# Optimization experiments

Measured on AMD Instinct MI355X. Metric: run time of the kernel, lower is better.

Reference implementation:

```python
import jax, jax.numpy as jnp
import numpy as np

N_ATOMS = 16384
APC = 64            # atoms per conformer
N_CONF = 256        # 64 mols * 4 confs
N_MOL = 64
DEG = 32
E = N_ATOMS * DEG
H = 128             # hidden_channels = num_filters = out_channels
G = 50              # num_gaussians
L = 6               # num_interactions
CUTOFF = 10.0
LOG2 = float(np.log(2.0))


def ssp(x):
    # ShiftedSoftplus: softplus(x) - log(2)
    return jax.nn.softplus(x) - LOG2


def setup_inputs() -> dict:
    key = jax.random.key(0)
    ks = jax.random.split(key, 24)
    rng = np.random.default_rng(0)

    z = jnp.asarray(rng.integers(1, 100, size=(N_ATOMS,)), dtype=jnp.int64 if jax.config.jax_enable_x64 else jnp.int32)
    # positions uniform in a 5A box -> all intra-conformer distances < cutoff
    pos = jax.random.uniform(ks[0], (N_ATOMS, 3), dtype=jnp.float32) * 5.0

    # within-conformer random edges, no self loops (radius_graph surrogate)
    i = np.repeat(np.arange(N_ATOMS), DEG)
    off = rng.integers(1, APC, size=E)
    j = (i // APC) * APC + (i % APC + off) % APC
    edge_index = jnp.asarray(np.stack([j, i]), dtype=jnp.int32)  # [2,E] (source, target)

    atom_to_conf = jnp.asarray(np.arange(N_ATOMS) // APC, dtype=jnp.int32)
    conf_to_mol = jnp.asarray(np.arange(N_CONF) // (N_CONF // N_MOL), dtype=jnp.int32)

    s = 0.05
    p = {
        'emb':     jax.random.normal(ks[1], (120, H), jnp.float32) * s,
        # per-interaction stacked params [L, ...]
        'mlp_w1':  jax.random.normal(ks[2], (L, G, H), jnp.float32) * s,
        'mlp_b1':  jnp.zeros((L, H), jnp.float32),
        'mlp_w2':  jax.random.normal(ks[3], (L, H, H), jnp.float32) * s,
        'mlp_b2':  jnp.zeros((L, H), jnp.float32),
        'cf_w1':   jax.random.normal(ks[4], (L, H, H), jnp.float32) * s,
        'cf_w2':   jax.random.normal(ks[5], (L, H, H), jnp.float32) * s,
        'cf_b2':   jnp.zeros((L, H), jnp.float32),
        'int_w':   jax.random.normal(ks[6], (L, H, H), jnp.float32) * s,
        'int_b':   jnp.zeros((L, H), jnp.float32),
        # readout head
        'out_w1':  jax.random.normal(ks[7], (H, H), jnp.float32) * s,
        'out_b1':  jnp.zeros((H,), jnp.float32),
        'out_w2':  jax.random.normal(ks[8], (H, H), jnp.float32) * s,
        'out_b2':  jnp.zeros((H,), jnp.float32),
        'head_w1': jax.random.normal(ks[9], (H, H // 2), jnp.float32) * s,
        'head_b1': jnp.zeros((H // 2,), jnp.float32),
        'head_w2': jax.random.normal(ks[10], (H // 2, 1), jnp.float32) * s,
        'head_b2': jnp.zeros((1,), jnp.float32),
    }
    return dict(z=z, pos=pos, edge_index=edge_index, atom_to_conf=atom_to_conf,
                conf_to_mol=conf_to_mol, **p)


def reference(z, pos, edge_index, atom_to_conf, conf_to_mol, emb,
              mlp_w1, mlp_b1, mlp_w2, mlp_b2, cf_w1, cf_w2, cf_b2,
              int_w, int_b, out_w1, out_b1, out_w2, out_b2,
              head_w1, head_b1, head_w2, head_b2):
    row, col = edge_index[0], edge_index[1]  # message from row, aggregated at col

    h = emb[z]                                             # [N,H]
    edge_weight = jnp.linalg.norm(pos[row] - pos[col], axis=-1)  # [E]

    # GaussianSmearing
    offset = jnp.linspace(0.0, CUTOFF, G)
    coeff = -0.5 / (offset[1] - offset[0]) ** 2
    edge_attr = jnp.exp(coeff * (edge_weight[:, None] - offset[None, :]) ** 2)  # [E,G]

    C = 0.5 * (jnp.cos(edge_weight * jnp.pi / CUTOFF) + 1.0)  # cosine cutoff [E]

    for l in range(L):
        # filter network on edge features, modulated by cutoff envelope
        Wf = ssp(edge_attr @ mlp_w1[l] + mlp_b1[l]) @ mlp_w2[l] + mlp_b2[l]
        Wf = Wf * C[:, None]                               # [E,H]
        xf = h @ cf_w1[l]                                  # lin1 (no bias) [N,H]
        msg = xf[row] * Wf                                 # gather * filter [E,H]
        agg = jax.ops.segment_sum(msg, col, num_segments=N_ATOMS)  # scatter-add [N,H]
        xc = agg @ cf_w2[l] + cf_b2[l]                     # lin2
        h = h + (ssp(xc) @ int_w[l] + int_b[l])            # act, lin, residual

    h = ssp(h @ out_w1 + out_b1)
    h = h @ out_w2 + out_b2                                # [N,H]

    conf_emb = jax.ops.segment_sum(h, atom_to_conf, num_segments=N_CONF)   # [C,H]
    mol_emb = jax.ops.segment_sum(conf_emb, conf_to_mol, num_segments=N_MOL)  # [M,H]

    out = (ssp(mol_emb @ head_w1 + head_b1) @ head_w2 + head_b2)[:, 0]  # [M]
    return out
```

## Files before the change

kernel.cpp:

```cpp
#include <hip/hip_runtime.h>
#include <math.h>

#define N_ATOMS 16384
#define APC 64
#define N_CONF 256
#define N_MOL 64
#define DEG 32
#define NEDGE (N_ATOMS * DEG)
#define H 128
#define G 50
#define NL 6
#define TP0 512
#define TPB 4096
#define CUTOFF 10.0f

typedef __attribute__((ext_vector_type(8))) short short8_t;
typedef __attribute__((ext_vector_type(4))) float f32x4;
typedef __attribute__((ext_vector_type(2))) float f32x2;

__device__ __forceinline__ float ssp_f(float x) {
  float e = __expf(-fabsf(x));
  return fmaxf(x, 0.f) + __logf(1.f + e) - 0.69314718055994531f;
}
__device__ __forceinline__ unsigned short bf16_rne(float x) {
  unsigned u = __float_as_uint(x);
  unsigned r = u + 0x7FFF + ((u >> 16) & 1);
  return (unsigned short)(r >> 16);
}
__device__ __forceinline__ float bf16_to_f(unsigned short s) {
  return __uint_as_float(((unsigned)s) << 16);
}
__device__ __forceinline__ float bflo(unsigned u) { return __uint_as_float(u << 16); }
__device__ __forceinline__ float bfhi(unsigned u) { return __uint_as_float(u & 0xFFFF0000u); }

__global__ __launch_bounds__(256) void k_setup(
    const float* __restrict__ pos, const int* __restrict__ esrc,
    const int* __restrict__ etgt, int* __restrict__ pk,
    const float* __restrict__ cf_w1, const float* __restrict__ cf_w2,
    const float* __restrict__ int_w, const float* __restrict__ out_w1,
    const float* __restrict__ out_w2, short* __restrict__ PW,
    const float* __restrict__ w1, const float* __restrict__ b1,
    const float* __restrict__ w2, const float* __restrict__ b2,
    float* __restrict__ T, int* __restrict__ cnt) {
  __shared__ float g2[2][64];
  __shared__ float S2[2][128];
  const int b = blockIdx.x;
  const int tid = threadIdx.x;
  if (b == 0 && tid == 0) *cnt = 0;
  if (b < 2048) {
    int e = b * 256 + tid;
    int r = esrc[e], c = etgt[e];
    float dx = pos[r * 3 + 0] - pos[c * 3 + 0];
    float dy = pos[r * 3 + 1] - pos[c * 3 + 1];
    float dz = pos[r * 3 + 2] - pos[c * 3 + 2];
    float d = sqrtf(dx * dx + dy * dy + dz * dz);
    int i = (int)(d * ((float)(TPB - 1) / CUTOFF) + 0.5f);
    if (i > TPB - 1) i = TPB - 1;
    if (i < 0) i = 0;
    pk[e] = (i << 8) | ((r & (APC - 1)) << 20);
  } else if (b < 2208) {
    int e = (b - 2048) * 256 + tid;
    int g = e >> 11, t = e & 2047;
    int kb = t >> 9, rem = t & 511, nt = rem >> 6, lane = rem & 63;
    int quad = lane >> 4, ln = lane & 15;
    int kbase = kb * 32 + quad * 8;
    int n = nt * 16 + ln;
    const float* src;
    if (g < 12) {
      int l = g >> 1;
      src = (g & 1) ? (int_w + l * 16384) : (cf_w2 + l * 16384);
    } else if (g < 18) {
      src = cf_w1 + (g - 12) * 16384;
    } else {
      src = (g == 18) ? out_w1 : out_w2;
    }
    short hv[8], lv[8];
    #pragma unroll
    for (int j = 0; j < 8; j++) {
      float x = src[(kbase + j) * H + n];
      unsigned short hb = bf16_rne(x);
      hv[j] = (short)hb;
      lv[j] = (short)bf16_rne(x - bf16_to_f(hb));
    }
    size_t base = (size_t)g * 32768 + (size_t)t * 8;
    *(short8_t*)&PW[base] = *(short8_t*)hv;
    *(short8_t*)&PW[base + 16384] = *(short8_t*)lv;
  } else {
    int bb = b - 2208;
    const int l = bb >> 8;
    const int grp = tid >> 7;
    const int c = tid & 127;
    const int p = (bb & 255) * 2 + grp;
    const float d = (float)p * (CUTOFF / (float)(TP0 - 1));
    const float gspace = CUTOFF / (float)(G - 1);
    const float coeff = -0.5f / (gspace * gspace);
    if (c < G) {
      float x = d - (float)c * gspace;
      g2[grp][c] = __expf(coeff * x * x);
    }
    __syncthreads();
    const float* W1 = w1 + l * G * H;
    float s = b1[l * H + c];
    #pragma unroll 5
    for (int i = 0; i < G; i++) s += g2[grp][i] * W1[i * H + c];
    S2[grp][c] = ssp_f(s);
    __syncthreads();
    const float* W2 = w2 + l * H * H;
    float o = b2[l * H + c];
    #pragma unroll 8
    for (int j = 0; j < H; j++) o += S2[grp][j] * W2[j * H + c];
    float Cc = 0.5f * (__cosf(d * (3.14159265358979f / CUTOFF)) + 1.f);
    T[((size_t)l * TP0 + p) * H + c] = o * Cc;
  }
}

__global__ __launch_bounds__(256) void k_up(const float* __restrict__ T,
                                            unsigned short* __restrict__ Tb) {
  int t = blockIdx.x * 256 + threadIdx.x;
  int l = t >> 17;
  int rem = t & 131071;
  int p4 = rem >> 5, cg = rem & 31;
  int c = cg * 4;
  float u = (float)p4 * ((float)(TP0 - 1) / (float)(TPB - 1));
  int i = (int)u;
  if (i > TP0 - 2) i = TP0 - 2;
  float f = u - (float)i;
  const float* a = T + ((size_t)l * TP0 + i) * H + c;
  float4 v0 = *(const float4*)a;
  float4 v1 = *(const float4*)(a + H);
  ushort4 o;
  o.x = bf16_rne(v0.x + f * (v1.x - v0.x));
  o.y = bf16_rne(v0.y + f * (v1.y - v0.y));
  o.z = bf16_rne(v0.z + f * (v1.z - v0.z));
  o.w = bf16_rne(v0.w + f * (v1.w - v0.w));
  *(ushort4*)&Tb[((size_t)l * TPB + p4) * H + c] = o;
}

#define MFMA(a, b, c) __builtin_amdgcn_mfma_f32_16x16x32_bf16((a), (b), (c), 0, 0, 0)

__device__ __forceinline__ void gemm_rt2(const short (*AH)[136], const short (*AL)[136],
                                         const short* __restrict__ pw,
                                         int rt2, int nt, int lane, int quad, int ln,
                                         f32x4 acc[2]) {
  #pragma unroll
  for (int kb = 0; kb < 4; kb++) {
    const short* pb = pw + ((size_t)(kb * 8 + nt) * 64 + lane) * 8;
    short8_t bh = *(const short8_t*)pb;
    short8_t bl = *(const short8_t*)(pb + 16384);
    int ko = kb * 32 + quad * 8;
    #pragma unroll
    for (int rtt = 0; rtt < 2; rtt++) {
      int row = rt2 * 32 + rtt * 16 + ln;
      short8_t ah = *(const short8_t*)&AH[row][ko];
      short8_t al = *(const short8_t*)&AL[row][ko];
      acc[rtt] = MFMA(ah, bh, acc[rtt]);
      acc[rtt] = MFMA(ah, bl, acc[rtt]);
      acc[rtt] = MFMA(al, bh, acc[rtt]);
    }
  }
}

__global__ __launch_bounds__(1024, 1) void k_mega(
    const int* __restrict__ z, const float* __restrict__ emb,
    const int* __restrict__ pk, const unsigned short* __restrict__ Tb,
    const short* __restrict__ PW, const float* __restrict__ cf_b2,
    const float* __restrict__ int_b, const float* __restrict__ out_b1,
    const float* __restrict__ out_b2, float* __restrict__ ce,
    const float* __restrict__ hw1, const float* __restrict__ hb1,
    const float* __restrict__ hw2, const float* __restrict__ hb2,
    int* __restrict__ cnt, float* __restrict__ outp) {
  __shared__ float xs[64][132];
  __shared__ __align__(16) short hH[64][136], hL[64][136];
  __shared__ __align__(16) short tH[64][136], tL[64][136];
  __shared__ __align__(16) short S1H[64][136], S1L[64][136];
  __shared__ int pks[2048];
  __shared__ float ps[2][128];
  __shared__ int is_last;
  const int conf = blockIdx.x;
  const int tid = threadIdx.x;
  const int lane = tid & 63, w = tid >> 6;
  const int quad = lane >> 4, ln = lane & 15;
  const int rt2 = w & 1, nt = w >> 1;
  const int eg = lane >> 4, ch0 = (lane & 15) * 8;

  pks[tid] = pk[conf * 2048 + tid];
  pks[tid + 1024] = pk[conf * 2048 + 1024 + tid];

  {
    int r = tid >> 4, cb = (tid & 15) * 8;
    const float* src = emb + (size_t)z[conf * 64 + r] * H + cb;
    float4 v0 = *(const float4*)src, v1 = *(const float4*)(src + 4);
    float vv[8] = {v0.x, v0.y, v0.z, v0.w, v1.x, v1.y, v1.z, v1.w};
    short hv[8], lv[8];
    #pragma unroll
    for (int u = 0; u < 8; u++) {
      unsigned short hb = bf16_rne(vv[u]);
      hv[u] = (short)hb;
      lv[u] = (short)bf16_rne(vv[u] - bf16_to_f(hb));
    }
    *(short8_t*)&hH[r][cb] = *(short8_t*)hv;
    *(short8_t*)&hL[r][cb] = *(short8_t*)lv;
  }
  __syncthreads();

  {
    f32x4 acc[2] = {{0.f, 0.f, 0.f, 0.f}, {0.f, 0.f, 0.f, 0.f}};
    gemm_rt2(hH, hL, PW + (size_t)12 * 32768, rt2, nt, lane, quad, ln, acc);
    int col = nt * 16 + ln;
    #pragma unroll
    for (int rtt = 0; rtt < 2; rtt++)
      #pragma unroll
      for (int reg = 0; reg < 4; reg++)
        xs[rt2 * 32 + rtt * 16 + quad * 4 + reg][col] = acc[rtt][reg];
  }
  __syncthreads();

  for (int l = 0; l < NL; l++) {
    const char* Tlb = (const char*)(Tb + (size_t)l * TPB * H) + ch0 * 2;
    #pragma unroll 1
    for (int aa = 0; aa < 4; aa++) {
      int a2 = w * 4 + aa;
      int ms[8];
      uint4 tvv[8];
      #pragma unroll
      for (int it = 0; it < 8; it++) {
        ms[it] = pks[a2 * DEG + it * 4 + eg];
        tvv[it] = *(const uint4*)(Tlb + (ms[it] & 0xFFFFF));
      }
      f32x2 ac0 = {0.f, 0.f}, ac1 = {0.f, 0.f}, ac2 = {0.f, 0.f}, ac3 = {0.f, 0.f};
      #pragma unroll
      for (int it = 0; it < 8; it++) {
        int sl = ms[it] >> 20;
        const float* xr = &xs[sl][ch0];
        float4 x0 = *(const float4*)xr;
        float4 x1 = *(const float4*)(xr + 4);
        uint4 tv = tvv[it];
        ac0 = __builtin_elementwise_fma((f32x2){bflo(tv.x), bfhi(tv.x)},
                                        (f32x2){x0.x, x0.y}, ac0);
        ac1 = __builtin_elementwise_fma((f32x2){bflo(tv.y), bfhi(tv.y)},
                                        (f32x2){x0.z, x0.w}, ac1);
        ac2 = __builtin_elementwise_fma((f32x2){bflo(tv.z), bfhi(tv.z)},
                                        (f32x2){x1.x, x1.y}, ac2);
        ac3 = __builtin_elementwise_fma((f32x2){bflo(tv.w), bfhi(tv.w)},
                                        (f32x2){x1.z, x1.w}, ac3);
      }
      float accs[8] = {ac0.x, ac0.y, ac1.x, ac1.y, ac2.x, ac2.y, ac3.x, ac3.y};
      #pragma unroll
      for (int j = 0; j < 8; j++) {
        accs[j] += __shfl_xor(accs[j], 16);
        accs[j] += __shfl_xor(accs[j], 32);
      }
      float va = eg == 0 ? accs[0] : eg == 1 ? accs[2] : eg == 2 ? accs[4] : accs[6];
      float vb = eg == 0 ? accs[1] : eg == 1 ? accs[3] : eg == 2 ? accs[5] : accs[7];
      unsigned short ha = bf16_rne(va), hb = bf16_rne(vb);
      unsigned short la = bf16_rne(va - bf16_to_f(ha));
      unsigned short lb = bf16_rne(vb - bf16_to_f(hb));
      int cw = ch0 + eg * 2;
      *(short2*)&S1H[a2][cw] = make_short2((short)ha, (short)hb);
      *(short2*)&S1L[a2][cw] = make_short2((short)la, (short)lb);
    }
    __syncthreads();
    {
      f32x4 acc[2] = {{0.f, 0.f, 0.f, 0.f}, {0.f, 0.f, 0.f, 0.f}};
      gemm_rt2(S1H, S1L, PW + (size_t)(2 * l) * 32768, rt2, nt, lane, quad, ln, acc);
      int col = nt * 16 + ln;
      float bb = cf_b2[l * H + col];
      #pragma unroll
      for (int rtt = 0; rtt < 2; rtt++)
        #pragma unroll
        for (int reg = 0; reg < 4; reg++) {
          int row = rt2 * 32 + rtt * 16 + quad * 4 + reg;
          float v = ssp_f(acc[rtt][reg] + bb);
          unsigned short hb = bf16_rne(v);
          tH[row][col] = (short)hb;
          tL[row][col] = (short)bf16_rne(v - bf16_to_f(hb));
        }
    }
    __syncthreads();
    {
      f32x4 acc[2] = {{0.f, 0.f, 0.f, 0.f}, {0.f, 0.f, 0.f, 0.f}};
      gemm_rt2(tH, tL, PW + (size_t)(2 * l + 1) * 32768, rt2, nt, lane, quad, ln, acc);
      int col = nt * 16 + ln;
      float bb = int_b[l * H + col];
      #pragma unroll
      for (int rtt = 0; rtt < 2; rtt++)
        #pragma unroll
        for (int reg = 0; reg < 4; reg++) {
          int row = rt2 * 32 + rtt * 16 + quad * 4 + reg;
          float hv = bf16_to_f((unsigned short)hH[row][col]) +
                     bf16_to_f((unsigned short)hL[row][col]);
          float v = acc[rtt][reg] + bb + hv;
          unsigned short hb = bf16_rne(v);
          hH[row][col] = (short)hb;
          hL[row][col] = (short)bf16_rne(v - bf16_to_f(hb));
        }
    }
    __syncthreads();
    if (l < NL - 1) {
      f32x4 acc[2] = {{0.f, 0.f, 0.f, 0.f}, {0.f, 0.f, 0.f, 0.f}};
      gemm_rt2(hH, hL, PW + (size_t)(13 + l) * 32768, rt2, nt, lane, quad, ln, acc);
      int col = nt * 16 + ln;
      #pragma unroll
      for (int rtt = 0; rtt < 2; rtt++)
        #pragma unroll
        for (int reg = 0; reg < 4; reg++)
          xs[rt2 * 32 + rtt * 16 + quad * 4 + reg][col] = acc[rtt][reg];
      __syncthreads();
    }
  }

  {
    f32x4 acc[2] = {{0.f, 0.f, 0.f, 0.f}, {0.f, 0.f, 0.f, 0.f}};
    gemm_rt2(hH, hL, PW + (size_t)18 * 32768, rt2, nt, lane, quad, ln, acc);
    int col = nt * 16 + ln;
    float bb = out_b1[col];
    #pragma unroll
    for (int rtt = 0; rtt < 2; rtt++)
      #pragma unroll
      for (int reg = 0; reg < 4; reg++) {
        int row = rt2 * 32 + rtt * 16 + quad * 4 + reg;
        float v = ssp_f(acc[rtt][reg] + bb);
        unsigned short hb = bf16_rne(v);
        tH[row][col] = (short)hb;
        tL[row][col] = (short)bf16_rne(v - bf16_to_f(hb));
      }
  }
  __syncthreads();
  {
    f32x4 acc[2] = {{0.f, 0.f, 0.f, 0.f}, {0.f, 0.f, 0.f, 0.f}};
    gemm_rt2(tH, tL, PW + (size_t)19 * 32768, rt2, nt, lane, quad, ln, acc);
    int col = nt * 16 + ln;
    float s = acc[0][0] + acc[0][1] + acc[0][2] + acc[0][3] +
              acc[1][0] + acc[1][1] + acc[1][2] + acc[1][3];
    s += __shfl_xor(s, 16);
    s += __shfl_xor(s, 32);
    if (quad == 0) ps[rt2][col] = s;
  }
  __syncthreads();
  if (tid < 128) {
    float v = ps[0][tid] + ps[1][tid] + 64.f * out_b2[tid];
    __hip_atomic_store(&ce[conf * 128 + tid], v, __ATOMIC_RELAXED,
                       __HIP_MEMORY_SCOPE_AGENT);
  }
  __syncthreads();
  if (tid == 0) {
    __threadfence();
    int old = __hip_atomic_fetch_add(cnt, 1, __ATOMIC_ACQ_REL,
                                     __HIP_MEMORY_SCOPE_AGENT);
    is_last = (old == N_CONF - 1) ? 1 : 0;
  }
  __syncthreads();
  if (is_last) {
    __threadfence();
    float* mol = &xs[0][0];
    for (int t = tid; t < N_MOL * 128; t += 1024) {
      int m = t >> 7, c = t & 127;
      const float* b = ce + (size_t)(m * 4) * 128;
      float s = __hip_atomic_load(&b[c], __ATOMIC_RELAXED, __HIP_MEMORY_SCOPE_AGENT) +
                __hip_atomic_load(&b[128 + c], __ATOMIC_RELAXED, __HIP_MEMORY_SCOPE_AGENT) +
                __hip_atomic_load(&b[256 + c], __ATOMIC_RELAXED, __HIP_MEMORY_SCOPE_AGENT) +
                __hip_atomic_load(&b[384 + c], __ATOMIC_RELAXED, __HIP_MEMORY_SCOPE_AGENT);
      mol[t] = s;
    }
    __syncthreads();
    float* q = (float*)&S1H[0][0];
    for (int t = tid; t < N_MOL * 64; t += 1024) {
      int m = t >> 6, j = t & 63;
      float qq = hb1[j];
      #pragma unroll 8
      for (int c = 0; c < H; c++) qq += mol[m * 128 + c] * hw1[c * 64 + j];
      q[t] = ssp_f(qq);
    }
    __syncthreads();
    if (tid < N_MOL) {
      float o = hb2[0];
      #pragma unroll 8
      for (int j = 0; j < 64; j++) o += q[tid * 64 + j] * hw2[j];
      outp[tid] = o;
    }
  }
}

extern "C" void kernel_launch(void* const* d_in, const int* in_sizes, int n_in,
                              void* d_out, int out_size, void* d_ws, size_t ws_size,
                              hipStream_t stream) {
  const int*   z       = (const int*)d_in[0];
  const float* pos     = (const float*)d_in[1];
  const int*   eidx    = (const int*)d_in[2];
  const float* emb     = (const float*)d_in[5];
  const float* mlp_w1  = (const float*)d_in[6];
  const float* mlp_b1  = (const float*)d_in[7];
  const float* mlp_w2  = (const float*)d_in[8];
  const float* mlp_b2  = (const float*)d_in[9];
  const float* cf_w1   = (const float*)d_in[10];
  const float* cf_w2   = (const float*)d_in[11];
  const float* cf_b2   = (const float*)d_in[12];
  const float* int_w   = (const float*)d_in[13];
  const float* int_b   = (const float*)d_in[14];
  const float* out_w1  = (const float*)d_in[15];
  const float* out_b1  = (const float*)d_in[16];
  const float* out_w2  = (const float*)d_in[17];
  const float* out_b2  = (const float*)d_in[18];
  const float* head_w1 = (const float*)d_in[19];
  const float* head_b1 = (const float*)d_in[20];
  const float* head_w2 = (const float*)d_in[21];
  const float* head_b2 = (const float*)d_in[22];

  char* ws = (char*)d_ws;
  float*          T   = (float*)ws;
  unsigned short* Tb  = (unsigned short*)(ws + (size_t)NL * TP0 * H * 4);
  char*           p2  = (char*)Tb + (size_t)NL * TPB * H * 2;
  int*            pk  = (int*)p2;
  short*          PW  = (short*)(p2 + (size_t)NEDGE * 4);
  float*          ce  = (float*)((char*)PW + (size_t)20 * 32768 * 2);
  int*            cnt = (int*)((char*)ce + (size_t)N_CONF * H * 4);

  k_setup<<<3744, 256, 0, stream>>>(pos, eidx, eidx + NEDGE, pk,
                                    cf_w1, cf_w2, int_w, out_w1, out_w2, PW,
                                    mlp_w1, mlp_b1, mlp_w2, mlp_b2, T, cnt);
  k_up<<<(NL * TPB * H / 4) / 256, 256, 0, stream>>>(T, Tb);

  k_mega<<<N_CONF, 1024, 0, stream>>>(z, emb, pk, Tb, PW, cf_b2, int_b,
                                      out_b1, out_b2, ce,
                                      head_w1, head_b1, head_w2, head_b2,
                                      cnt, (float*)d_out);
}
```

Measured before the change: 239.6 us.

## Fuse table upsampling into setup, compute edge distances in mega kernel, retile GEMMs

Removes the separate upsample kernel: each setup block evaluates the few coarse filter-table points it needs into shared memory and writes the interpolated bf16 rows directly. Edge distance and packing move out of setup into the mega kernel, which reads conformer positions into shared memory and computes the bins locally, avoiding a global pk round-trip. The wave-to-tile mapping in the MFMA GEMMs changes from 2 row-tiles by 1 column-tile to 1 row-tile by 2 column-tiles, and the edge-gather channel layout changes to match. The cost is redundant MLP evaluation of overlapping coarse points across setup blocks and extra work at the start of the mega kernel.

```diff
diff --git a/kernel.cpp b/kernel.cpp
--- a/kernel.cpp
+++ b/kernel.cpp
@@ -13,6 +13,8 @@
 #define TP0 512
 #define TPB 4096
 #define CUTOFF 10.0f
+#define WBLK 160
+#define TBLK (NL * 256)
 
 typedef __attribute__((ext_vector_type(8))) short short8_t;
 typedef __attribute__((ext_vector_type(4))) float f32x4;
@@ -34,37 +36,25 @@
 __device__ __forceinline__ float bfhi(unsigned u) { return __uint_as_float(u & 0xFFFF0000u); }
 
 __global__ __launch_bounds__(256) void k_setup(
-    const float* __restrict__ pos, const int* __restrict__ esrc,
-    const int* __restrict__ etgt, int* __restrict__ pk,
     const float* __restrict__ cf_w1, const float* __restrict__ cf_w2,
     const float* __restrict__ int_w, const float* __restrict__ out_w1,
     const float* __restrict__ out_w2, short* __restrict__ PW,
     const float* __restrict__ w1, const float* __restrict__ b1,
     const float* __restrict__ w2, const float* __restrict__ b2,
-    float* __restrict__ T, int* __restrict__ cnt) {
-  __shared__ float g2[2][64];
+    unsigned short* __restrict__ Tb, int* __restrict__ cnt) {
+  __shared__ float g2s[2][64];
   __shared__ float S2[2][128];
+  __shared__ float OutS[4][132];
   const int b = blockIdx.x;
   const int tid = threadIdx.x;
   if (b == 0 && tid == 0) *cnt = 0;
-  if (b < 2048) {
+  if (b < WBLK) {
     int e = b * 256 + tid;
-    int r = esrc[e], c = etgt[e];
-    float dx = pos[r * 3 + 0] - pos[c * 3 + 0];
-    float dy = pos[r * 3 + 1] - pos[c * 3 + 1];
-    float dz = pos[r * 3 + 2] - pos[c * 3 + 2];
-    float d = sqrtf(dx * dx + dy * dy + dz * dz);
-    int i = (int)(d * ((float)(TPB - 1) / CUTOFF) + 0.5f);
-    if (i > TPB - 1) i = TPB - 1;
-    if (i < 0) i = 0;
-    pk[e] = (i << 8) | ((r & (APC - 1)) << 20);
-  } else if (b < 2208) {
-    int e = (b - 2048) * 256 + tid;
     int g = e >> 11, t = e & 2047;
     int kb = t >> 9, rem = t & 511, nt = rem >> 6, lane = rem & 63;
-    int quad = lane >> 4, ln = lane & 15;
+    int quad = lane >> 4, ln2 = lane & 15;
     int kbase = kb * 32 + quad * 8;
-    int n = nt * 16 + ln;
+    int n = nt * 16 + ln2;
     const float* src;
     if (g < 12) {
       int l = g >> 1;
@@ -86,83 +76,85 @@
     *(short8_t*)&PW[base] = *(short8_t*)hv;
     *(short8_t*)&PW[base + 16384] = *(short8_t*)lv;
   } else {
-    int bb = b - 2208;
-    const int l = bb >> 8;
-    const int grp = tid >> 7;
-    const int c = tid & 127;
-    const int p = (bb & 255) * 2 + grp;
-    const float d = (float)p * (CUTOFF / (float)(TP0 - 1));
+    int bb = b - WBLK;
+    const int l = bb >> 8, q = bb & 255;
+    const int grp = tid >> 7, c = tid & 127;
+    const int p_min =
+        (int)((float)(q * 16) * ((float)(TP0 - 1) / (float)(TPB - 1)));
     const float gspace = CUTOFF / (float)(G - 1);
     const float coeff = -0.5f / (gspace * gspace);
-    if (c < G) {
-      float x = d - (float)c * gspace;
-      g2[grp][c] = __expf(coeff * x * x);
-    }
-    __syncthreads();
     const float* W1 = w1 + l * G * H;
-    float s = b1[l * H + c];
-    #pragma unroll 5
-    for (int i = 0; i < G; i++) s += g2[grp][i] * W1[i * H + c];
-    S2[grp][c] = ssp_f(s);
-    __syncthreads();
     const float* W2 = w2 + l * H * H;
-    float o = b2[l * H + c];
-    #pragma unroll 8
-    for (int j = 0; j < H; j++) o += S2[grp][j] * W2[j * H + c];
-    float Cc = 0.5f * (__cosf(d * (3.14159265358979f / CUTOFF)) + 1.f);
-    T[((size_t)l * TP0 + p) * H + c] = o * Cc;
-  }
-}
-
-__global__ __launch_bounds__(256) void k_up(const float* __restrict__ T,
-                                            unsigned short* __restrict__ Tb) {
-  int t = blockIdx.x * 256 + threadIdx.x;
-  int l = t >> 17;
-  int rem = t & 131071;
-  int p4 = rem >> 5, cg = rem & 31;
-  int c = cg * 4;
-  float u = (float)p4 * ((float)(TP0 - 1) / (float)(TPB - 1));
-  int i = (int)u;
-  if (i > TP0 - 2) i = TP0 - 2;
-  float f = u - (float)i;
-  const float* a = T + ((size_t)l * TP0 + i) * H + c;
-  float4 v0 = *(const float4*)a;
-  float4 v1 = *(const float4*)(a + H);
-  ushort4 o;
-  o.x = bf16_rne(v0.x + f * (v1.x - v0.x));
-  o.y = bf16_rne(v0.y + f * (v1.y - v0.y));
-  o.z = bf16_rne(v0.z + f * (v1.z - v0.z));
-  o.w = bf16_rne(v0.w + f * (v1.w - v0.w));
-  *(ushort4*)&Tb[((size_t)l * TPB + p4) * H + c] = o;
+    #pragma unroll 1
+    for (int r = 0; r < 2; r++) {
+      int pt = r * 2 + grp;
+      int p = p_min + pt;
+      if (p > TP0 - 1) p = TP0 - 1;
+      float d = (float)p * (CUTOFF / (float)(TP0 - 1));
+      if (c < G) {
+        float x = d - (float)c * gspace;
+        g2s[grp][c] = __expf(coeff * x * x);
+      }
+      __syncthreads();
+      float s = b1[l * H + c];
+      #pragma unroll 5
+      for (int i = 0; i < G; i++) s += g2s[grp][i] * W1[i * H + c];
+      S2[grp][c] = ssp_f(s);
+      __syncthreads();
+      float o = b2[l * H + c];
+      #pragma unroll 8
+      for (int j = 0; j < H; j++) o += S2[grp][j] * W2[j * H + c];
+      float Cc = 0.5f * (__cosf(d * (3.14159265358979f / CUTOFF)) + 1.f);
+      OutS[pt][c] = o * Cc;
+      __syncthreads();
+    }
+    int p4o = tid >> 4, cg = tid & 15;
+    int p4 = q * 16 + p4o;
+    float u = (float)p4 * ((float)(TP0 - 1) / (float)(TPB - 1));
+    int i = (int)u;
+    if (i > TP0 - 2) i = TP0 - 2;
+    float f = u - (float)i;
+    int li = i - p_min;
+    short8_t ov;
+    #pragma unroll
+    for (int j = 0; j < 4; j++) {
+      float a0 = OutS[li][cg * 4 + j], a1 = OutS[li + 1][cg * 4 + j];
+      ov[j] = (short)bf16_rne(a0 + f * (a1 - a0));
+      float b0 = OutS[li][64 + cg * 4 + j], b1v = OutS[li + 1][64 + cg * 4 + j];
+      ov[4 + j] = (short)bf16_rne(b0 + f * (b1v - b0));
+    }
+    *(short8_t*)&Tb[((size_t)l * TPB + p4) * H + cg * 8] = ov;
+  }
 }
 
 #define MFMA(a, b, c) __builtin_amdgcn_mfma_f32_16x16x32_bf16((a), (b), (c), 0, 0, 0)
 
-__device__ __forceinline__ void gemm_rt2(const short (*AH)[136], const short (*AL)[136],
+__device__ __forceinline__ void gemm_1x2(const short (*AH)[136], const short (*AL)[136],
                                          const short* __restrict__ pw,
-                                         int rt2, int nt, int lane, int quad, int ln,
+                                         int rt, int ct2, int lane, int quad, int ln,
                                          f32x4 acc[2]) {
   #pragma unroll
   for (int kb = 0; kb < 4; kb++) {
-    const short* pb = pw + ((size_t)(kb * 8 + nt) * 64 + lane) * 8;
-    short8_t bh = *(const short8_t*)pb;
-    short8_t bl = *(const short8_t*)(pb + 16384);
     int ko = kb * 32 + quad * 8;
-    #pragma unroll
-    for (int rtt = 0; rtt < 2; rtt++) {
-      int row = rt2 * 32 + rtt * 16 + ln;
-      short8_t ah = *(const short8_t*)&AH[row][ko];
-      short8_t al = *(const short8_t*)&AL[row][ko];
-      acc[rtt] = MFMA(ah, bh, acc[rtt]);
-      acc[rtt] = MFMA(ah, bl, acc[rtt]);
-      acc[rtt] = MFMA(al, bh, acc[rtt]);
+    int row = rt * 16 + ln;
+    short8_t ah = *(const short8_t*)&AH[row][ko];
+    short8_t al = *(const short8_t*)&AL[row][ko];
+    #pragma unroll
+    for (int ct = 0; ct < 2; ct++) {
+      const short* pb = pw + ((size_t)(kb * 8 + ct2 * 2 + ct) * 64 + lane) * 8;
+      short8_t bh = *(const short8_t*)pb;
+      short8_t bl = *(const short8_t*)(pb + 16384);
+      acc[ct] = MFMA(ah, bh, acc[ct]);
+      acc[ct] = MFMA(ah, bl, acc[ct]);
+      acc[ct] = MFMA(al, bh, acc[ct]);
     }
   }
 }
 
 __global__ __launch_bounds__(1024, 1) void k_mega(
     const int* __restrict__ z, const float* __restrict__ emb,
-    const int* __restrict__ pk, const unsigned short* __restrict__ Tb,
+    const float* __restrict__ pos, const int* __restrict__ esrc,
+    const unsigned short* __restrict__ Tb,
     const short* __restrict__ PW, const float* __restrict__ cf_b2,
     const float* __restrict__ int_b, const float* __restrict__ out_b1,
     const float* __restrict__ out_b2, float* __restrict__ ce,
@@ -174,17 +166,17 @@
   __shared__ __align__(16) short tH[64][136], tL[64][136];
   __shared__ __align__(16) short S1H[64][136], S1L[64][136];
   __shared__ int pks[2048];
-  __shared__ float ps[2][128];
+  __shared__ float ps[4][128];
   __shared__ int is_last;
   const int conf = blockIdx.x;
   const int tid = threadIdx.x;
   const int lane = tid & 63, w = tid >> 6;
   const int quad = lane >> 4, ln = lane & 15;
-  const int rt2 = w & 1, nt = w >> 1;
-  const int eg = lane >> 4, ch0 = (lane & 15) * 8;
-
-  pks[tid] = pk[conf * 2048 + tid];
-  pks[tid + 1024] = pk[conf * 2048 + 1024 + tid];
+  const int rt = w & 3, ct2 = w >> 2;
+  const int eg = lane >> 4, c0 = (lane & 15) * 4;
+
+  float* posl = &xs[0][0];
+  if (tid < 192) posl[tid] = pos[conf * 192 + tid];
 
   {
     int r = tid >> 4, cb = (tid & 15) * 8;
@@ -203,20 +195,37 @@
   }
   __syncthreads();
 
+  #pragma unroll
+  for (int e0 = 0; e0 < 2; e0++) {
+    int e = e0 * 1024 + tid;
+    int s = esrc[conf * 2048 + e] & (APC - 1);
+    int t = e >> 5;
+    float dx = posl[s * 3 + 0] - posl[t * 3 + 0];
+    float dy = posl[s * 3 + 1] - posl[t * 3 + 1];
+    float dz = posl[s * 3 + 2] - posl[t * 3 + 2];
+    float d = sqrtf(dx * dx + dy * dy + dz * dz);
+    int i = (int)(d * ((float)(TPB - 1) / CUTOFF) + 0.5f);
+    if (i > TPB - 1) i = TPB - 1;
+    if (i < 0) i = 0;
+    pks[e] = (i << 8) | (s << 20);
+  }
+  __syncthreads();
+
   {
     f32x4 acc[2] = {{0.f, 0.f, 0.f, 0.f}, {0.f, 0.f, 0.f, 0.f}};
-    gemm_rt2(hH, hL, PW + (size_t)12 * 32768, rt2, nt, lane, quad, ln, acc);
-    int col = nt * 16 + ln;
-    #pragma unroll
-    for (int rtt = 0; rtt < 2; rtt++)
+    gemm_1x2(hH, hL, PW + (size_t)12 * 32768, rt, ct2, lane, quad, ln, acc);
+    #pragma unroll
+    for (int ct = 0; ct < 2; ct++) {
+      int col = (ct2 * 2 + ct) * 16 + ln;
       #pragma unroll
       for (int reg = 0; reg < 4; reg++)
-        xs[rt2 * 32 + rtt * 16 + quad * 4 + reg][col] = acc[rtt][reg];
+        xs[rt * 16 + quad * 4 + reg][col] = acc[ct][reg];
+    }
   }
   __syncthreads();
 
   for (int l = 0; l < NL; l++) {
-    const char* Tlb = (const char*)(Tb + (size_t)l * TPB * H) + ch0 * 2;
+    const char* Tlb = (const char*)(Tb + (size_t)l * TPB * H) + ln * 16;
     #pragma unroll 1
     for (int aa = 0; aa < 4; aa++) {
       int a2 = w * 4 + aa;
@@ -231,9 +240,9 @@
       #pragma unroll
       for (int it = 0; it < 8; it++) {
         int sl = ms[it] >> 20;
-        const float* xr = &xs[sl][ch0];
+        const float* xr = &xs[sl][c0];
         float4 x0 = *(const float4*)xr;
-        float4 x1 = *(const float4*)(xr + 4);
+        float4 x1 = *(const float4*)(xr + 64);
         uint4 tv = tvv[it];
         ac0 = __builtin_elementwise_fma((f32x2){bflo(tv.x), bfhi(tv.x)},
                                         (f32x2){x0.x, x0.y}, ac0);
@@ -255,90 +264,97 @@
       unsigned short ha = bf16_rne(va), hb = bf16_rne(vb);
       unsigned short la = bf16_rne(va - bf16_to_f(ha));
       unsigned short lb = bf16_rne(vb - bf16_to_f(hb));
-      int cw = ch0 + eg * 2;
+      int cw = (eg >> 1) * 64 + c0 + (eg & 1) * 2;
       *(short2*)&S1H[a2][cw] = make_short2((short)ha, (short)hb);
       *(short2*)&S1L[a2][cw] = make_short2((short)la, (short)lb);
     }
     __syncthreads();
     {
       f32x4 acc[2] = {{0.f, 0.f, 0.f, 0.f}, {0.f, 0.f, 0.f, 0.f}};
-      gemm_rt2(S1H, S1L, PW + (size_t)(2 * l) * 32768, rt2, nt, lane, quad, ln, acc);
-      int col = nt * 16 + ln;
-      float bb = cf_b2[l * H + col];
-      #pragma unroll
-      for (int rtt = 0; rtt < 2; rtt++)
+      gemm_1x2(S1H, S1L, PW + (size_t)(2 * l) * 32768, rt, ct2, lane, quad, ln, acc);
+      #pragma unroll
+      for (int ct = 0; ct < 2; ct++) {
+        int col = (ct2 * 2 + ct) * 16 + ln;
+        float bb = cf_b2[l * H + col];
         #pragma unroll
         for (int reg = 0; reg < 4; reg++) {
-          int row = rt2 * 32 + rtt * 16 + quad * 4 + reg;
-          float v = ssp_f(acc[rtt][reg] + bb);
+          int row = rt * 16 + quad * 4 + reg;
+          float v = ssp_f(acc[ct][reg] + bb);
           unsigned short hb = bf16_rne(v);
           tH[row][col] = (short)hb;
           tL[row][col] = (short)bf16_rne(v - bf16_to_f(hb));
         }
+      }
     }
     __syncthreads();
     {
       f32x4 acc[2] = {{0.f, 0.f, 0.f, 0.f}, {0.f, 0.f, 0.f, 0.f}};
-      gemm_rt2(tH, tL, PW + (size_t)(2 * l + 1) * 32768, rt2, nt, lane, quad, ln, acc);
-      int col = nt * 16 + ln;
-      float bb = int_b[l * H + col];
-      #pragma unroll
-      for (int rtt = 0; rtt < 2; rtt++)
+      gemm_1x2(tH, tL, PW + (size_t)(2 * l + 1) * 32768, rt, ct2, lane, quad, ln, acc);
+      #pragma unroll
+      for (int ct = 0; ct < 2; ct++) {
+        int col = (ct2 * 2 + ct) * 16 + ln;
+        float bb = int_b[l * H + col];
         #pragma unroll
         for (int reg = 0; reg < 4; reg++) {
-          int row = rt2 * 32 + rtt * 16 + quad * 4 + reg;
+          int row = rt * 16 + quad * 4 + reg;
           float hv = bf16_to_f((unsigned short)hH[row][col]) +
                      bf16_to_f((unsigned short)hL[row][col]);
-          float v = acc[rtt][reg] + bb + hv;
+          float v = acc[ct][reg] + bb + hv;
           unsigned short hb = bf16_rne(v);
           hH[row][col] = (short)hb;
           hL[row][col] = (short)bf16_rne(v - bf16_to_f(hb));
         }
+      }
     }
     __syncthreads();
     if (l < NL - 1) {
       f32x4 acc[2] = {{0.f, 0.f, 0.f, 0.f}, {0.f, 0.f, 0.f, 0.f}};
-      gemm_rt2(hH, hL, PW + (size_t)(13 + l) * 32768, rt2, nt, lane, quad, ln, acc);
-      int col = nt * 16 + ln;
-      #pragma unroll
-      for (int rtt = 0; rtt < 2; rtt++)
+      gemm_1x2(hH, hL, PW + (size_t)(13 + l) * 32768, rt, ct2, lane, quad, ln, acc);
+      #pragma unroll
+      for (int ct = 0; ct < 2; ct++) {
+        int col = (ct2 * 2 + ct) * 16 + ln;
         #pragma unroll
         for (int reg = 0; reg < 4; reg++)
-          xs[rt2 * 32 + rtt * 16 + quad * 4 + reg][col] = acc[rtt][reg];
+          xs[rt * 16 + quad * 4 + reg][col] = acc[ct][reg];
+      }
       __syncthreads();
     }
   }
 
   {
     f32x4 acc[2] = {{0.f, 0.f, 0.f, 0.f}, {0.f, 0.f, 0.f, 0.f}};
-    gemm_rt2(hH, hL, PW + (size_t)18 * 32768, rt2, nt, lane, quad, ln, acc);
-    int col = nt * 16 + ln;
-    float bb = out_b1[col];
-    #pragma unroll
-    for (int rtt = 0; rtt < 2; rtt++)
+    gemm_1x2(hH, hL, PW + (size_t)18 * 32768, rt, ct2, lane, quad, ln, acc);
+    #pragma unroll
+    for (int ct = 0; ct < 2; ct++) {
+      int col = (ct2 * 2 + ct) * 16 + ln;
+      float bb = out_b1[col];
       #pragma unroll
       for (int reg = 0; reg < 4; reg++) {
-        int row = rt2 * 32 + rtt * 16 + quad * 4 + reg;
-        float v = ssp_f(acc[rtt][reg] + bb);
+        int row = rt * 16 + quad * 4 + reg;
+        float v = ssp_f(acc[ct][reg] + bb);
         unsigned short hb = bf16_rne(v);
         tH[row][col] = (short)hb;
         tL[row][col] = (short)bf16_rne(v - bf16_to_f(hb));
       }
+    }
   }
   __syncthreads();
   {
     f32x4 acc[2] = {{0.f, 0.f, 0.f, 0.f}, {0.f, 0.f, 0.f, 0.f}};
-    gemm_rt2(tH, tL, PW + (size_t)19 * 32768, rt2, nt, lane, quad, ln, acc);
-    int col = nt * 16 + ln;
-    float s = acc[0][0] + acc[0][1] + acc[0][2] + acc[0][3] +
-              acc[1][0] + acc[1][1] + acc[1][2] + acc[1][3];
-    s += __shfl_xor(s, 16);
-    s += __shfl_xor(s, 32);
-    if (quad == 0) ps[rt2][col] = s;
+    gemm_1x2(tH, tL, PW + (size_t)19 * 32768, rt, ct2, lane, quad, ln, acc);
+    #pragma unroll
+    for (int ct = 0; ct < 2; ct++) {
+      int col = (ct2 * 2 + ct) * 16 + ln;
+      float s = acc[ct][0] + acc[ct][1] + acc[ct][2] + acc[ct][3];
+      s += __shfl_xor(s, 16);
+      s += __shfl_xor(s, 32);
+      if (quad == 0) ps[rt][col] = s;
+    }
   }
   __syncthreads();
   if (tid < 128) {
-    float v = ps[0][tid] + ps[1][tid] + 64.f * out_b2[tid];
+    float v = ps[0][tid] + ps[1][tid] + ps[2][tid] + ps[3][tid] +
+              64.f * out_b2[tid];
     __hip_atomic_store(&ce[conf * 128 + tid], v, __ATOMIC_RELAXED,
                        __HIP_MEMORY_SCOPE_AGENT);
   }
@@ -407,20 +423,16 @@
   const float* head_b2 = (const float*)d_in[22];
 
   char* ws = (char*)d_ws;
-  float*          T   = (float*)ws;
-  unsigned short* Tb  = (unsigned short*)(ws + (size_t)NL * TP0 * H * 4);
-  char*           p2  = (char*)Tb + (size_t)NL * TPB * H * 2;
-  int*            pk  = (int*)p2;
-  short*          PW  = (short*)(p2 + (size_t)NEDGE * 4);
-  float*          ce  = (float*)((char*)PW + (size_t)20 * 32768 * 2);
-  int*            cnt = (int*)((char*)ce + (size_t)N_CONF * H * 4);
-
-  k_setup<<<3744, 256, 0, stream>>>(pos, eidx, eidx + NEDGE, pk,
-                                    cf_w1, cf_w2, int_w, out_w1, out_w2, PW,
-                                    mlp_w1, mlp_b1, mlp_w2, mlp_b2, T, cnt);
-  k_up<<<(NL * TPB * H / 4) / 256, 256, 0, stream>>>(T, Tb);
-
-  k_mega<<<N_CONF, 1024, 0, stream>>>(z, emb, pk, Tb, PW, cf_b2, int_b,
+  unsigned short* Tb = (unsigned short*)ws;
+  short* PW  = (short*)(ws + (size_t)NL * TPB * H * 2);
+  float* ce  = (float*)((char*)PW + (size_t)20 * 32768 * 2);
+  int*   cnt = (int*)((char*)ce + (size_t)N_CONF * H * 4);
+
+  k_setup<<<WBLK + TBLK, 256, 0, stream>>>(cf_w1, cf_w2, int_w, out_w1, out_w2,
+                                           PW, mlp_w1, mlp_b1, mlp_w2, mlp_b2,
+                                           Tb, cnt);
+
+  k_mega<<<N_CONF, 1024, 0, stream>>>(z, emb, pos, eidx, Tb, PW, cf_b2, int_b,
                                       out_b1, out_b2, ce,
                                       head_w1, head_b1, head_w2, head_b2,
                                       cnt, (float*)d_out);
```

Result: slower. 262.9 us (+9.7%).
